# Kernel tuning notes

Measured on AMD Instinct MI355X. Metric: run time of the kernel, lower is better.

The kernel has to match this reference:

```python
import jax, jax.numpy as jnp
import numpy as np

B, S, D_MODEL, N_HEADS, D_K, D_V = 4, 1024, 1024, 16, 64, 64
LN_EPS = 1e-5


def setup_inputs() -> dict:
    key = jax.random.key(0)
    ks = jax.random.split(key, 10)
    inp = {
        "input_Q": jax.random.normal(ks[0], (B, S, D_MODEL), dtype=jnp.float32),
        "input_K": jax.random.normal(ks[1], (B, S, D_MODEL), dtype=jnp.float32),
        "input_V": jax.random.normal(ks[2], (B, S, D_MODEL), dtype=jnp.float32),
        "attn_mask": jax.random.randint(ks[3], (B, S, S), 0, 2) > 0,
        "res_att": jax.random.normal(ks[4], (B, N_HEADS, S, S), dtype=jnp.float32),
        # weights stored as [in, out] (torch Linear applies x @ W.T)
        "W_Q": jax.random.normal(ks[5], (D_MODEL, N_HEADS * D_K), dtype=jnp.float32) * 0.02,
        "W_K": jax.random.normal(ks[6], (D_MODEL, N_HEADS * D_K), dtype=jnp.float32) * 0.02,
        "W_V": jax.random.normal(ks[7], (D_MODEL, N_HEADS * D_V), dtype=jnp.float32) * 0.02,
        "W_fc": jax.random.normal(ks[8], (N_HEADS * D_V, D_MODEL), dtype=jnp.float32) * 0.02,
        "ln_gamma": jnp.ones((D_MODEL,), dtype=jnp.float32),
        "ln_beta": jnp.zeros((D_MODEL,), dtype=jnp.float32),
    }
    return inp


def layer_norm(x, gamma, beta):
    mu = jnp.mean(x, axis=-1, keepdims=True)
    var = jnp.mean((x - mu) ** 2, axis=-1, keepdims=True)
    return (x - mu) * jax.lax.rsqrt(var + LN_EPS) * gamma + beta


def reference(input_Q, input_K, input_V, attn_mask, res_att,
              W_Q, W_K, W_V, W_fc, ln_gamma, ln_beta):
    b, s, _ = input_Q.shape
    residual = input_Q
    # project and split heads: [B, H, S, d]
    Q = (input_Q @ W_Q).reshape(b, s, N_HEADS, D_K).transpose(0, 2, 1, 3)
    K = (input_K @ W_K).reshape(b, -1, N_HEADS, D_K).transpose(0, 2, 1, 3)
    V = (input_V @ W_V).reshape(b, -1, N_HEADS, D_V).transpose(0, 2, 1, 3)
    # scores [B, H, Sq, Sk] + residual attention bias
    scores = jnp.einsum("bhqd,bhkd->bhqk", Q, K) / np.sqrt(D_K).astype(np.float32)
    scores = scores + res_att
    scores = jnp.where(attn_mask[:, None, :, :], jnp.float32(-1e9), scores)
    attn = jax.nn.softmax(scores, axis=-1)
    context = jnp.einsum("bhqk,bhkd->bhqd", attn, V)
    context = context.transpose(0, 2, 1, 3).reshape(b, s, N_HEADS * D_V)
    output = context @ W_fc
    out = layer_norm(output + residual, ln_gamma, ln_beta)
    return (out, attn)
```

## Files before the change

### kernel.cpp

```cpp
#include <hip/hip_runtime.h>


typedef short short8 __attribute__((ext_vector_type(8)));
typedef float f32x4 __attribute__((ext_vector_type(4)));

__device__ __forceinline__ unsigned short f2bf(float f) {
  unsigned int u = __float_as_uint(f);
  u += 0x7fffu + ((u >> 16) & 1u);
  return (unsigned short)(u >> 16);
}

__global__ __launch_bounds__(256) void cvt3_kernel(
    const float* __restrict__ a, const float* __restrict__ b, const float* __restrict__ c,
    unsigned short* __restrict__ oa, unsigned short* __restrict__ ob, unsigned short* __restrict__ oc)
{
  const float* src = blockIdx.y == 0 ? a : (blockIdx.y == 1 ? b : c);
  unsigned short* dst = blockIdx.y == 0 ? oa : (blockIdx.y == 1 ? ob : oc);
  size_t i = (size_t)blockIdx.x * 256 + threadIdx.x;
  float4 v = ((const float4*)src)[i];
  ushort4 o;
  o.x = f2bf(v.x); o.y = f2bf(v.y); o.z = f2bf(v.z); o.w = f2bf(v.w);
  ((ushort4*)dst)[i] = o;
}

__global__ void wtrans_kernel(
    const float* __restrict__ w0, const float* __restrict__ w1,
    const float* __restrict__ w2, const float* __restrict__ w3,
    unsigned short* __restrict__ o0, unsigned short* __restrict__ o1,
    unsigned short* __restrict__ o2, unsigned short* __restrict__ o3)
{
  __shared__ float tile[32][33];
  int z = blockIdx.z;
  const float* src = z == 0 ? w0 : (z == 1 ? w1 : (z == 2 ? w2 : w3));
  unsigned short* dst = z == 0 ? o0 : (z == 1 ? o1 : (z == 2 ? o2 : o3));
  int bx = blockIdx.x * 32;
  int by = blockIdx.y * 32;
  int tx = threadIdx.x, ty = threadIdx.y;
#pragma unroll
  for (int i = 0; i < 4; ++i)
    tile[ty + 8 * i][tx] = src[(size_t)(by + ty + 8 * i) * 1024 + bx + tx];
  __syncthreads();
#pragma unroll
  for (int i = 0; i < 4; ++i)
    dst[(size_t)(bx + ty + 8 * i) * 1024 + by + tx] = f2bf(tile[tx][ty + 8 * i]);
}

__device__ __forceinline__ void gemm_core(const unsigned short* __restrict__ A,
                                          const unsigned short* __restrict__ Bt,
                                          int m0, int n0, f32x4 (&acc)[4][4])
{
  __shared__ unsigned short As[128][40];
  __shared__ unsigned short Bs[128][40];
  const int tid = threadIdx.x;
  const int lane = tid & 63;
  const int w = tid >> 6;
  const int wm = (w >> 1) << 6;
  const int wn = (w & 1) << 6;
  const int lr = lane & 15;
  const int lk = (lane >> 4) << 3;

  f32x4 zero = {0.f, 0.f, 0.f, 0.f};
#pragma unroll
  for (int mi = 0; mi < 4; ++mi)
#pragma unroll
    for (int ni = 0; ni < 4; ++ni) acc[mi][ni] = zero;

  for (int kt = 0; kt < 1024; kt += 32) {
    __syncthreads();
#pragma unroll
    for (int i = 0; i < 2; ++i) {
      int c = tid + (i << 8);
      int r = c >> 2, ko = (c & 3) << 3;
      *(short8*)&As[r][ko] = *(const short8*)&A[(size_t)(m0 + r) * 1024 + kt + ko];
      *(short8*)&Bs[r][ko] = *(const short8*)&Bt[(size_t)(n0 + r) * 1024 + kt + ko];
    }
    __syncthreads();
    short8 a[4], b[4];
#pragma unroll
    for (int mi = 0; mi < 4; ++mi) a[mi] = *(const short8*)&As[wm + mi * 16 + lr][lk];
#pragma unroll
    for (int ni = 0; ni < 4; ++ni) b[ni] = *(const short8*)&Bs[wn + ni * 16 + lr][lk];
#pragma unroll
    for (int mi = 0; mi < 4; ++mi)
#pragma unroll
      for (int ni = 0; ni < 4; ++ni)
        acc[mi][ni] = __builtin_amdgcn_mfma_f32_16x16x32_bf16(a[mi], b[ni], acc[mi][ni], 0, 0, 0);
  }
}

__global__ __launch_bounds__(256) void proj_gemm(
    const unsigned short* __restrict__ Xq, const unsigned short* __restrict__ Xk,
    const unsigned short* __restrict__ Xv,
    const unsigned short* __restrict__ Wtq, const unsigned short* __restrict__ Wtk,
    const unsigned short* __restrict__ Wtv,
    unsigned short* __restrict__ Qp, unsigned short* __restrict__ Kp,
    unsigned short* __restrict__ Vpt)
{
  const int mode = blockIdx.z;
  const unsigned short* A = mode == 0 ? Xq : (mode == 1 ? Xk : Xv);
  const unsigned short* Bt = mode == 0 ? Wtq : (mode == 1 ? Wtk : Wtv);
  const int m0 = blockIdx.y * 128;
  const int n0 = blockIdx.x * 128;

  f32x4 acc[4][4];
  gemm_core(A, Bt, m0, n0, acc);

  const int lane = threadIdx.x & 63;
  const int w = threadIdx.x >> 6;
  const int wm = (w >> 1) << 6;
  const int wn = (w & 1) << 6;
  const int lr = lane & 15;
  const int lg = lane >> 4;
  const float scale = (mode == 0) ? 0.125f : 1.0f;
  unsigned short* dst01 = (mode == 0) ? Qp : Kp;

#pragma unroll
  for (int mi = 0; mi < 4; ++mi)
#pragma unroll
    for (int ni = 0; ni < 4; ++ni)
#pragma unroll
      for (int r = 0; r < 4; ++r) {
        int m = m0 + wm + mi * 16 + (lg << 2) + r;
        int n = n0 + wn + ni * 16 + lr;
        float v = acc[mi][ni][r] * scale;
        int bb = m >> 10, ss = m & 1023, hh = n >> 6, dd = n & 63;
        if (mode < 2)
          dst01[((((size_t)bb * 16 + hh) << 10) + ss) * 64 + dd] = f2bf(v);
        else
          Vpt[((((size_t)bb * 16 + hh) * 64 + dd) << 10) + ss] = f2bf(v);
      }
}

__global__ __launch_bounds__(256) void fc_gemm(
    const unsigned short* __restrict__ Ctx, const unsigned short* __restrict__ Wtf,
    float* __restrict__ OutLin)
{
  const int m0 = blockIdx.y * 128;
  const int n0 = blockIdx.x * 128;
  f32x4 acc[4][4];
  gemm_core(Ctx, Wtf, m0, n0, acc);

  const int lane = threadIdx.x & 63;
  const int w = threadIdx.x >> 6;
  const int wm = (w >> 1) << 6;
  const int wn = (w & 1) << 6;
  const int lr = lane & 15;
  const int lg = lane >> 4;
#pragma unroll
  for (int mi = 0; mi < 4; ++mi)
#pragma unroll
    for (int ni = 0; ni < 4; ++ni)
#pragma unroll
      for (int r = 0; r < 4; ++r) {
        int m = m0 + wm + mi * 16 + (lg << 2) + r;
        int n = n0 + wn + ni * 16 + lr;
        OutLin[(size_t)m * 1024 + n] = acc[mi][ni][r];
      }
}

__global__ __launch_bounds__(256) void attn_kernel(
    const unsigned short* __restrict__ Qp, const unsigned short* __restrict__ Kp,
    const unsigned short* __restrict__ Vpt,
    const float* __restrict__ res_att, const int* __restrict__ mask,
    float* __restrict__ attn_out, unsigned short* __restrict__ Ctx)
{
  __shared__ float Slds[16][1024];
  const int qb = blockIdx.x, h = blockIdx.y, b = blockIdx.z;
  const int q0 = qb * 16;
  const int tid = threadIdx.x;
  const int lane = tid & 63;
  const int w = tid >> 6;
  const int lr = lane & 15;
  const int lg = lane >> 4;
  const int lk = lg << 3;

  const unsigned short* Qbh = Qp + (((size_t)b * 16 + h) << 16);
  const unsigned short* Kbh = Kp + (((size_t)b * 16 + h) << 16);
  const unsigned short* Vbh = Vpt + (((size_t)b * 16 + h) << 16);
  const float* res_row = res_att + ((((size_t)b * 16 + h) * 1024 + q0) << 10);
  const int* msk_row = mask + ((((size_t)b) * 1024 + q0) << 10);
  float* attn_row = attn_out + ((((size_t)b * 16 + h) * 1024 + q0) << 10);

  short8 aq0 = *(const short8*)&Qbh[(size_t)(q0 + lr) * 64 + lk];
  short8 aq1 = *(const short8*)&Qbh[(size_t)(q0 + lr) * 64 + 32 + lk];

  f32x4 zero = {0.f, 0.f, 0.f, 0.f};
#pragma unroll 1
  for (int t = 0; t < 16; ++t) {
    int n0 = (w * 16 + t) * 16;
    short8 bk0 = *(const short8*)&Kbh[(size_t)(n0 + lr) * 64 + lk];
    short8 bk1 = *(const short8*)&Kbh[(size_t)(n0 + lr) * 64 + 32 + lk];
    f32x4 acc = zero;
    acc = __builtin_amdgcn_mfma_f32_16x16x32_bf16(aq0, bk0, acc, 0, 0, 0);
    acc = __builtin_amdgcn_mfma_f32_16x16x32_bf16(aq1, bk1, acc, 0, 0, 0);
    int col = n0 + lr;
#pragma unroll
    for (int r = 0; r < 4; ++r) {
      int row = (lg << 2) + r;
      float sv = acc[r] + res_row[((size_t)row << 10) + col];
      if (msk_row[((size_t)row << 10) + col] != 0) sv = -1e9f;
      Slds[row][col ^ ((row & 7) << 2)] = sv;
    }
  }
  __syncthreads();

  for (int r = w; r < 16; r += 4) {
    int swz = (r & 7) << 2;
    float v[16];
    float mx = -1e30f;
#pragma unroll
    for (int i = 0; i < 16; ++i) {
      v[i] = Slds[r][(lane + (i << 6)) ^ swz];
      mx = fmaxf(mx, v[i]);
    }
#pragma unroll
    for (int off = 32; off >= 1; off >>= 1) mx = fmaxf(mx, __shfl_xor(mx, off));
    float sum = 0.f;
#pragma unroll
    for (int i = 0; i < 16; ++i) { v[i] = __expf(v[i] - mx); sum += v[i]; }
#pragma unroll
    for (int off = 32; off >= 1; off >>= 1) sum += __shfl_xor(sum, off);
    float inv = 1.f / sum;
#pragma unroll
    for (int i = 0; i < 16; ++i) {
      float p = v[i] * inv;
      Slds[r][(lane + (i << 6)) ^ swz] = p;
      attn_row[((size_t)r << 10) + lane + (i << 6)] = p;
    }
  }
  __syncthreads();

  f32x4 co = zero;
  const int dv0 = w * 16;
  const int swz = (lr & 7) << 2;
#pragma unroll 1
  for (int ks = 0; ks < 32; ++ks) {
    int k0 = (ks << 5) + lk;
    const float* srow = &Slds[lr][0];
    float4 f0 = *(const float4*)&srow[k0 ^ swz];
    float4 f1 = *(const float4*)&srow[(k0 + 4) ^ swz];
    short8 pa;
    pa[0] = (short)f2bf(f0.x); pa[1] = (short)f2bf(f0.y);
    pa[2] = (short)f2bf(f0.z); pa[3] = (short)f2bf(f0.w);
    pa[4] = (short)f2bf(f1.x); pa[5] = (short)f2bf(f1.y);
    pa[6] = (short)f2bf(f1.z); pa[7] = (short)f2bf(f1.w);
    short8 bv = *(const short8*)&Vbh[(size_t)(dv0 + lr) * 1024 + (ks << 5) + lk];
    co = __builtin_amdgcn_mfma_f32_16x16x32_bf16(pa, bv, co, 0, 0, 0);
  }
#pragma unroll
  for (int r = 0; r < 4; ++r) {
    int row = (lg << 2) + r;
    int dv = dv0 + lr;
    Ctx[((size_t)(b * 1024 + q0 + row)) * 1024 + h * 64 + dv] = f2bf(co[r]);
  }
}

__global__ __launch_bounds__(256) void ln_kernel(
    const float* __restrict__ xlin, const float* __restrict__ resid,
    const float* __restrict__ gamma, const float* __restrict__ beta,
    float* __restrict__ out)
{
  const int m = blockIdx.x;
  const int t = threadIdx.x;
  float4 v = ((const float4*)(xlin + ((size_t)m << 10)))[t];
  float4 rq = ((const float4*)(resid + ((size_t)m << 10)))[t];
  v.x += rq.x; v.y += rq.y; v.z += rq.z; v.w += rq.w;
  float s = v.x + v.y + v.z + v.w;
  float s2 = v.x * v.x + v.y * v.y + v.z * v.z + v.w * v.w;
#pragma unroll
  for (int off = 32; off >= 1; off >>= 1) {
    s += __shfl_xor(s, off);
    s2 += __shfl_xor(s2, off);
  }
  __shared__ float rs[4], rs2[4];
  const int w = t >> 6, lane = t & 63;
  if (lane == 0) { rs[w] = s; rs2[w] = s2; }
  __syncthreads();
  s = rs[0] + rs[1] + rs[2] + rs[3];
  s2 = rs2[0] + rs2[1] + rs2[2] + rs2[3];
  float mu = s * (1.f / 1024.f);
  float var = s2 * (1.f / 1024.f) - mu * mu;
  float rstd = rsqrtf(var + 1e-5f);
  float4 g = ((const float4*)gamma)[t];
  float4 bt = ((const float4*)beta)[t];
  float4 o;
  o.x = (v.x - mu) * rstd * g.x + bt.x;
  o.y = (v.y - mu) * rstd * g.y + bt.y;
  o.z = (v.z - mu) * rstd * g.z + bt.z;
  o.w = (v.w - mu) * rstd * g.w + bt.w;
  ((float4*)(out + ((size_t)m << 10)))[t] = o;
}

extern "C" void kernel_launch(void* const* d_in, const int* in_sizes, int n_in,
                              void* d_out, int out_size, void* d_ws, size_t ws_size,
                              hipStream_t stream) {
  const float* inQ = (const float*)d_in[0];
  const float* inK = (const float*)d_in[1];
  const float* inV = (const float*)d_in[2];
  const int* msk = (const int*)d_in[3];
  const float* res = (const float*)d_in[4];
  const float* wq = (const float*)d_in[5];
  const float* wk = (const float*)d_in[6];
  const float* wv = (const float*)d_in[7];
  const float* wfc = (const float*)d_in[8];
  const float* gamma = (const float*)d_in[9];
  const float* beta = (const float*)d_in[10];

  unsigned short* Xq = (unsigned short*)d_ws;
  unsigned short* Xk = Xq + 4194304;
  unsigned short* Xv = Xk + 4194304;
  unsigned short* Wtq = Xv + 4194304;
  unsigned short* Wtk = Wtq + 1048576;
  unsigned short* Wtv = Wtk + 1048576;
  unsigned short* Wtf = Wtv + 1048576;
  unsigned short* Qp = Wtf + 1048576;
  unsigned short* Kp = Qp + 4194304;
  unsigned short* Vpt = Kp + 4194304;
  unsigned short* Ctx = Vpt + 4194304;
  float* OutLin = (float*)d_ws;

  float* out = (float*)d_out;
  float* attn_out = out + 4194304;

  cvt3_kernel<<<dim3(4096, 3, 1), 256, 0, stream>>>(inQ, inK, inV, Xq, Xk, Xv);
  wtrans_kernel<<<dim3(32, 32, 4), dim3(32, 8, 1), 0, stream>>>(wq, wk, wv, wfc, Wtq, Wtk, Wtv, Wtf);
  proj_gemm<<<dim3(8, 32, 3), 256, 0, stream>>>(Xq, Xk, Xv, Wtq, Wtk, Wtv, Qp, Kp, Vpt);
  attn_kernel<<<dim3(64, 16, 4), 256, 0, stream>>>(Qp, Kp, Vpt, res, msk, attn_out, Ctx);
  fc_gemm<<<dim3(8, 32, 1), 256, 0, stream>>>(Ctx, Wtf, OutLin);
  ln_kernel<<<dim3(4096, 1, 1), 256, 0, stream>>>(OutLin, inQ, gamma, beta, out);
}
```

Measured before the change: 369.2 us.

## Store scores as fp16 in LDS and vectorize res_att/mask loads in softmax

The attention kernel now keeps raw QK scores as fp16 in shared memory, halving LDS use from 64KB to 32KB. The res_att and mask reads move from scattered scalar loads in the MFMA loop to coalesced float4/int4 loads in the softmax phase, and the attn output is written as float4. Probabilities are stored back as bf16, so the PV MFMA loads operands directly without per-step conversion. The smaller LDS footprint may allow more resident blocks. The cost is precision loss from rounding the raw scores to fp16 before the bias is added.

Result: faster. 324.9 us (-12.0%).

```diff
diff --git a/kernel.cpp b/kernel.cpp
--- a/kernel.cpp
+++ b/kernel.cpp
@@ -1,7 +1,9 @@
 #include <hip/hip_runtime.h>
+#include <hip/hip_fp16.h>
 
 
 typedef short short8 __attribute__((ext_vector_type(8)));
+typedef unsigned short ushort8 __attribute__((ext_vector_type(8)));
 typedef float f32x4 __attribute__((ext_vector_type(4)));
 
 __device__ __forceinline__ unsigned short f2bf(float f) {
@@ -164,7 +166,7 @@
     const float* __restrict__ res_att, const int* __restrict__ mask,
     float* __restrict__ attn_out, unsigned short* __restrict__ Ctx)
 {
-  __shared__ float Slds[16][1024];
+  __shared__ unsigned short S16[16 * 1024];
   const int qb = blockIdx.x, h = blockIdx.y, b = blockIdx.z;
   const int q0 = qb * 16;
   const int tid = threadIdx.x;
@@ -185,7 +187,7 @@
   short8 aq1 = *(const short8*)&Qbh[(size_t)(q0 + lr) * 64 + 32 + lk];
 
   f32x4 zero = {0.f, 0.f, 0.f, 0.f};
-#pragma unroll 1
+#pragma unroll 2
   for (int t = 0; t < 16; ++t) {
     int n0 = (w * 16 + t) * 16;
     short8 bk0 = *(const short8*)&Kbh[(size_t)(n0 + lr) * 64 + lk];
@@ -197,61 +199,84 @@
 #pragma unroll
     for (int r = 0; r < 4; ++r) {
       int row = (lg << 2) + r;
-      float sv = acc[r] + res_row[((size_t)row << 10) + col];
-      if (msk_row[((size_t)row << 10) + col] != 0) sv = -1e9f;
-      Slds[row][col ^ ((row & 7) << 2)] = sv;
+      int idx = row * 1024 + ((((col >> 3) ^ (row & 7)) << 3) | (col & 7));
+      S16[idx] = __half_as_ushort(__float2half(acc[r]));
     }
   }
   __syncthreads();
 
+#pragma unroll 1
   for (int r = w; r < 16; r += 4) {
-    int swz = (r & 7) << 2;
-    float v[16];
-    float mx = -1e30f;
-#pragma unroll
-    for (int i = 0; i < 16; ++i) {
-      v[i] = Slds[r][(lane + (i << 6)) ^ swz];
-      mx = fmaxf(mx, v[i]);
+    const int swz = r & 7;
+    const unsigned short* srow = &S16[r * 1024];
+    ushort8 hv0 = *(const ushort8*)&srow[(lane ^ swz) << 3];
+    ushort8 hv1 = *(const ushort8*)&srow[((64 + lane) ^ swz) << 3];
+    const float4* res4 = (const float4*)(res_row + ((size_t)r << 10));
+    const int4* msk4 = (const int4*)(msk_row + ((size_t)r << 10));
+    float4 ra = res4[lane * 2],       rb = res4[lane * 2 + 1];
+    float4 rc = res4[128 + lane * 2], rd = res4[128 + lane * 2 + 1];
+    int4 ma = msk4[lane * 2],       mb = msk4[lane * 2 + 1];
+    int4 mc = msk4[128 + lane * 2], md = msk4[128 + lane * 2 + 1];
+
+    float sv[16];
+    {
+      const float4 rs_[4] = {ra, rb, rc, rd};
+      const int4 ms_[4] = {ma, mb, mc, md};
+#pragma unroll
+      for (int g = 0; g < 4; ++g) {
+        ushort8 hv = (g < 2) ? hv0 : hv1;
+        int base = (g & 1) << 2;
+#pragma unroll
+        for (int e = 0; e < 4; ++e) {
+          float s = __half2float(__ushort_as_half(hv[base + e]));
+          float rr = (&rs_[g].x)[e];
+          int mm = (&ms_[g].x)[e];
+          sv[g * 4 + e] = mm ? -1e9f : s + rr;
+        }
+      }
     }
+    float mx = sv[0];
+#pragma unroll
+    for (int i = 1; i < 16; ++i) mx = fmaxf(mx, sv[i]);
 #pragma unroll
     for (int off = 32; off >= 1; off >>= 1) mx = fmaxf(mx, __shfl_xor(mx, off));
     float sum = 0.f;
 #pragma unroll
-    for (int i = 0; i < 16; ++i) { v[i] = __expf(v[i] - mx); sum += v[i]; }
+    for (int i = 0; i < 16; ++i) { sv[i] = __expf(sv[i] - mx); sum += sv[i]; }
 #pragma unroll
     for (int off = 32; off >= 1; off >>= 1) sum += __shfl_xor(sum, off);
     float inv = 1.f / sum;
 #pragma unroll
-    for (int i = 0; i < 16; ++i) {
-      float p = v[i] * inv;
-      Slds[r][(lane + (i << 6)) ^ swz] = p;
-      attn_row[((size_t)r << 10) + lane + (i << 6)] = p;
-    }
+    for (int i = 0; i < 16; ++i) sv[i] *= inv;
+
+    float4* att4 = (float4*)(attn_row + ((size_t)r << 10));
+    att4[lane * 2]       = make_float4(sv[0], sv[1], sv[2], sv[3]);
+    att4[lane * 2 + 1]   = make_float4(sv[4], sv[5], sv[6], sv[7]);
+    att4[128 + lane * 2] = make_float4(sv[8], sv[9], sv[10], sv[11]);
+    att4[128 + lane * 2 + 1] = make_float4(sv[12], sv[13], sv[14], sv[15]);
+
+    ushort8 pb0, pb1;
+#pragma unroll
+    for (int e = 0; e < 8; ++e) { pb0[e] = f2bf(sv[e]); pb1[e] = f2bf(sv[8 + e]); }
+    *(ushort8*)&S16[r * 1024 + ((lane ^ swz) << 3)] = pb0;
+    *(ushort8*)&S16[r * 1024 + (((64 + lane) ^ swz) << 3)] = pb1;
   }
   __syncthreads();
 
   f32x4 co = zero;
   const int dv0 = w * 16;
-  const int swz = (lr & 7) << 2;
-#pragma unroll 1
+  const int pswz = lr & 7;
+#pragma unroll 2
   for (int ks = 0; ks < 32; ++ks) {
-    int k0 = (ks << 5) + lk;
-    const float* srow = &Slds[lr][0];
-    float4 f0 = *(const float4*)&srow[k0 ^ swz];
-    float4 f1 = *(const float4*)&srow[(k0 + 4) ^ swz];
-    short8 pa;
-    pa[0] = (short)f2bf(f0.x); pa[1] = (short)f2bf(f0.y);
-    pa[2] = (short)f2bf(f0.z); pa[3] = (short)f2bf(f0.w);
-    pa[4] = (short)f2bf(f1.x); pa[5] = (short)f2bf(f1.y);
-    pa[6] = (short)f2bf(f1.z); pa[7] = (short)f2bf(f1.w);
+    int u = (ks << 2) + lg;
+    short8 pa = *(const short8*)&S16[lr * 1024 + ((u ^ pswz) << 3)];
     short8 bv = *(const short8*)&Vbh[(size_t)(dv0 + lr) * 1024 + (ks << 5) + lk];
     co = __builtin_amdgcn_mfma_f32_16x16x32_bf16(pa, bv, co, 0, 0, 0);
   }
 #pragma unroll
   for (int r = 0; r < 4; ++r) {
     int row = (lg << 2) + r;
-    int dv = dv0 + lr;
-    Ctx[((size_t)(b * 1024 + q0 + row)) * 1024 + h * 64 + dv] = f2bf(co[r]);
+    Ctx[((size_t)(b * 1024 + q0 + row)) * 1024 + h * 64 + dv0 + lr] = f2bf(co[r]);
   }
 }
 
```

## Restructure attention kernel with fp16 score LDS and vectorized nontemporal bias/mask I/O

Applied to the files above, without the earlier changes.

Raw QK scores are now stored to shared memory as fp16 instead of fp32, halving LDS use from 64KB to 32KB. The bias add and masking move into the softmax phase, where res_att and mask are read as coalesced 16-byte vectors and res_att rows are prefetched with nontemporal loads that overlap with processing. Probabilities are written out with vectorized nontemporal stores and kept in LDS as bf16, so the PV MFMA loop reads its operands directly without per-element conversion. Rounding QK scores to fp16 before the bias add loses precision, and the lower LDS footprint may raise occupancy.

Result: faster. 314.6 us (-14.8%).

```diff
diff --git a/kernel.cpp b/kernel.cpp
--- a/kernel.cpp
+++ b/kernel.cpp
@@ -1,14 +1,20 @@
 #include <hip/hip_runtime.h>
+#include <hip/hip_fp16.h>
 
 
 typedef short short8 __attribute__((ext_vector_type(8)));
+typedef unsigned short ushort8 __attribute__((ext_vector_type(8)));
 typedef float f32x4 __attribute__((ext_vector_type(4)));
+typedef int i32x4 __attribute__((ext_vector_type(4)));
 
 __device__ __forceinline__ unsigned short f2bf(float f) {
   unsigned int u = __float_as_uint(f);
   u += 0x7fffu + ((u >> 16) & 1u);
   return (unsigned short)(u >> 16);
 }
+
+#define BAR() do { asm volatile("s_waitcnt lgkmcnt(0)" ::: "memory"); \
+                   __builtin_amdgcn_s_barrier(); } while (0)
 
 __global__ __launch_bounds__(256) void cvt3_kernel(
     const float* __restrict__ a, const float* __restrict__ b, const float* __restrict__ c,
@@ -164,7 +170,7 @@
     const float* __restrict__ res_att, const int* __restrict__ mask,
     float* __restrict__ attn_out, unsigned short* __restrict__ Ctx)
 {
-  __shared__ float Slds[16][1024];
+  __shared__ unsigned short S16[16 * 1024];
   const int qb = blockIdx.x, h = blockIdx.y, b = blockIdx.z;
   const int q0 = qb * 16;
   const int tid = threadIdx.x;
@@ -185,7 +191,7 @@
   short8 aq1 = *(const short8*)&Qbh[(size_t)(q0 + lr) * 64 + 32 + lk];
 
   f32x4 zero = {0.f, 0.f, 0.f, 0.f};
-#pragma unroll 1
+#pragma unroll 2
   for (int t = 0; t < 16; ++t) {
     int n0 = (w * 16 + t) * 16;
     short8 bk0 = *(const short8*)&Kbh[(size_t)(n0 + lr) * 64 + lk];
@@ -197,61 +203,96 @@
 #pragma unroll
     for (int r = 0; r < 4; ++r) {
       int row = (lg << 2) + r;
-      float sv = acc[r] + res_row[((size_t)row << 10) + col];
-      if (msk_row[((size_t)row << 10) + col] != 0) sv = -1e9f;
-      Slds[row][col ^ ((row & 7) << 2)] = sv;
+      int idx = row * 1024 + ((((col >> 3) ^ (row & 7)) << 3) | (col & 7));
+      S16[idx] = __half_as_ushort(__float2half(acc[r]));
     }
   }
-  __syncthreads();
-
-  for (int r = w; r < 16; r += 4) {
-    int swz = (r & 7) << 2;
-    float v[16];
-    float mx = -1e30f;
-#pragma unroll
-    for (int i = 0; i < 16; ++i) {
-      v[i] = Slds[r][(lane + (i << 6)) ^ swz];
-      mx = fmaxf(mx, v[i]);
-    }
-#pragma unroll
-    for (int off = 32; off >= 1; off >>= 1) mx = fmaxf(mx, __shfl_xor(mx, off));
-    float sum = 0.f;
-#pragma unroll
-    for (int i = 0; i < 16; ++i) { v[i] = __expf(v[i] - mx); sum += v[i]; }
-#pragma unroll
-    for (int off = 32; off >= 1; off >>= 1) sum += __shfl_xor(sum, off);
-    float inv = 1.f / sum;
-#pragma unroll
-    for (int i = 0; i < 16; ++i) {
-      float p = v[i] * inv;
-      Slds[r][(lane + (i << 6)) ^ swz] = p;
-      attn_row[((size_t)r << 10) + lane + (i << 6)] = p;
-    }
-  }
-  __syncthreads();
+
+#define LOAD_RES(R, P0, P1, P2, P3)                                          \
+  do {                                                                        \
+    const f32x4* res4_ = (const f32x4*)(res_row + ((size_t)(R) << 10));       \
+    P0 = __builtin_nontemporal_load(&res4_[lane * 2]);                        \
+    P1 = __builtin_nontemporal_load(&res4_[lane * 2 + 1]);                    \
+    P2 = __builtin_nontemporal_load(&res4_[128 + lane * 2]);                  \
+    P3 = __builtin_nontemporal_load(&res4_[128 + lane * 2 + 1]);              \
+  } while (0)
+
+  f32x4 pa0, pa1, pa2, pa3, pb0, pb1, pb2, pb3;
+  f32x4 pc0, pc1, pc2, pc3, pd0, pd1, pd2, pd3;
+  LOAD_RES(w, pa0, pa1, pa2, pa3);
+  LOAD_RES(w + 4, pb0, pb1, pb2, pb3);
+
+  BAR();
+
+#define PROC_ROW(R, P0, P1, P2, P3)                                              \
+  do {                                                                            \
+    const int r_ = (R);                                                           \
+    const int swz_ = r_ & 7;                                                      \
+    ushort8 hv0 = *(const ushort8*)&S16[r_ * 1024 + ((lane ^ swz_) << 3)];        \
+    ushort8 hv1 = *(const ushort8*)&S16[r_ * 1024 + (((64 + lane) ^ swz_) << 3)]; \
+    const i32x4* msk4_ = (const i32x4*)(msk_row + ((size_t)r_ << 10));            \
+    i32x4 ma = msk4_[lane * 2], mb = msk4_[lane * 2 + 1];                         \
+    i32x4 mc = msk4_[128 + lane * 2], md = msk4_[128 + lane * 2 + 1];             \
+    float sv[16];                                                                 \
+    _Pragma("unroll")                                                             \
+    for (int e = 0; e < 4; ++e) {                                                 \
+      sv[e]      = ma[e] ? -1e9f : __half2float(__ushort_as_half(hv0[e]))     + P0[e]; \
+      sv[4 + e]  = mb[e] ? -1e9f : __half2float(__ushort_as_half(hv0[4 + e])) + P1[e]; \
+      sv[8 + e]  = mc[e] ? -1e9f : __half2float(__ushort_as_half(hv1[e]))     + P2[e]; \
+      sv[12 + e] = md[e] ? -1e9f : __half2float(__ushort_as_half(hv1[4 + e])) + P3[e]; \
+    }                                                                             \
+    float mx = sv[0];                                                             \
+    _Pragma("unroll")                                                             \
+    for (int i = 1; i < 16; ++i) mx = fmaxf(mx, sv[i]);                           \
+    _Pragma("unroll")                                                             \
+    for (int off = 32; off >= 1; off >>= 1) mx = fmaxf(mx, __shfl_xor(mx, off));  \
+    float sum = 0.f;                                                              \
+    _Pragma("unroll")                                                             \
+    for (int i = 0; i < 16; ++i) { sv[i] = __expf(sv[i] - mx); sum += sv[i]; }    \
+    _Pragma("unroll")                                                             \
+    for (int off = 32; off >= 1; off >>= 1) sum += __shfl_xor(sum, off);          \
+    float inv = 1.f / sum;                                                        \
+    _Pragma("unroll")                                                             \
+    for (int i = 0; i < 16; ++i) sv[i] *= inv;                                    \
+    f32x4* att4_ = (f32x4*)(attn_row + ((size_t)r_ << 10));                       \
+    f32x4 o0_ = {sv[0], sv[1], sv[2], sv[3]};                                     \
+    f32x4 o1_ = {sv[4], sv[5], sv[6], sv[7]};                                     \
+    f32x4 o2_ = {sv[8], sv[9], sv[10], sv[11]};                                   \
+    f32x4 o3_ = {sv[12], sv[13], sv[14], sv[15]};                                 \
+    __builtin_nontemporal_store(o0_, &att4_[lane * 2]);                           \
+    __builtin_nontemporal_store(o1_, &att4_[lane * 2 + 1]);                       \
+    __builtin_nontemporal_store(o2_, &att4_[128 + lane * 2]);                     \
+    __builtin_nontemporal_store(o3_, &att4_[128 + lane * 2 + 1]);                 \
+    ushort8 q0_, q1_;                                                             \
+    _Pragma("unroll")                                                             \
+    for (int e = 0; e < 8; ++e) { q0_[e] = f2bf(sv[e]); q1_[e] = f2bf(sv[8 + e]); } \
+    *(ushort8*)&S16[r_ * 1024 + ((lane ^ swz_) << 3)] = q0_;                      \
+    *(ushort8*)&S16[r_ * 1024 + (((64 + lane) ^ swz_) << 3)] = q1_;               \
+  } while (0)
+
+  PROC_ROW(w, pa0, pa1, pa2, pa3);
+  LOAD_RES(w + 8, pc0, pc1, pc2, pc3);
+  PROC_ROW(w + 4, pb0, pb1, pb2, pb3);
+  LOAD_RES(w + 12, pd0, pd1, pd2, pd3);
+  PROC_ROW(w + 8, pc0, pc1, pc2, pc3);
+  PROC_ROW(w + 12, pd0, pd1, pd2, pd3);
+
+  BAR();
 
   f32x4 co = zero;
   const int dv0 = w * 16;
-  const int swz = (lr & 7) << 2;
-#pragma unroll 1
+  const int pswz = lr & 7;
+#pragma unroll 4
   for (int ks = 0; ks < 32; ++ks) {
-    int k0 = (ks << 5) + lk;
-    const float* srow = &Slds[lr][0];
-    float4 f0 = *(const float4*)&srow[k0 ^ swz];
-    float4 f1 = *(const float4*)&srow[(k0 + 4) ^ swz];
-    short8 pa;
-    pa[0] = (short)f2bf(f0.x); pa[1] = (short)f2bf(f0.y);
-    pa[2] = (short)f2bf(f0.z); pa[3] = (short)f2bf(f0.w);
-    pa[4] = (short)f2bf(f1.x); pa[5] = (short)f2bf(f1.y);
-    pa[6] = (short)f2bf(f1.z); pa[7] = (short)f2bf(f1.w);
+    int u = (ks << 2) + lg;
+    short8 pa = *(const short8*)&S16[lr * 1024 + ((u ^ pswz) << 3)];
     short8 bv = *(const short8*)&Vbh[(size_t)(dv0 + lr) * 1024 + (ks << 5) + lk];
     co = __builtin_amdgcn_mfma_f32_16x16x32_bf16(pa, bv, co, 0, 0, 0);
   }
 #pragma unroll
   for (int r = 0; r < 4; ++r) {
     int row = (lg << 2) + r;
-    int dv = dv0 + lr;
-    Ctx[((size_t)(b * 1024 + q0 + row)) * 1024 + h * 64 + dv] = f2bf(co[r]);
+    Ctx[((size_t)(b * 1024 + q0 + row)) * 1024 + h * 64 + dv0 + lr] = f2bf(co[r]);
   }
 }
 
```
